# Optimization experiments

Measured on AMD Instinct MI355X. Metric: run time of the kernel, lower is better.

## Reference

```python
import jax, jax.numpy as jnp
import numpy as np

B, L_DEC, L_ENC = 4, 1024, 1024
D_MODEL, D_INNER, N_HEAD, D_K, D_V = 512, 256, 8, 64, 64
TEMP = D_K ** 0.5
EPS = 1e-6


def _layernorm(x, g, b):
    mu = jnp.mean(x, axis=-1, keepdims=True)
    var = jnp.mean(jnp.square(x - mu), axis=-1, keepdims=True)
    return (x - mu) * jax.lax.rsqrt(var + EPS) * g + b


def _mha(x_q, x_kv, Wq, Wk, Wv, Wfc, ln_g, ln_b, mask):
    # Faithful to source: only the query input is layer-normed; k/v use raw x_kv.
    resid = x_q
    qn = _layernorm(x_q, ln_g, ln_b)
    # Stacked per-head projections: Wq/Wk/Wv are [H, d_k, d_model]
    q = jnp.einsum('bld,hkd->bhlk', qn, Wq) / TEMP   # [B,H,Lq,dk]
    k = jnp.einsum('bld,hkd->bhlk', x_kv, Wk)        # [B,H,Lk,dk]
    v = jnp.einsum('bld,hkd->bhlk', x_kv, Wv)        # [B,H,Lk,dv]
    scores = jnp.einsum('bhqd,bhkd->bhqk', q, k)     # [B,H,Lq,Lk]
    if mask is not None:
        scores = jnp.where(mask[:, None, :, :] == 0, -jnp.inf, scores)
    attn = jax.nn.softmax(scores, axis=-1)
    out = jnp.einsum('bhqk,bhkd->bhqd', attn, v)     # [B,H,Lq,dv]
    Bq, H, Lq, dv = out.shape
    out = out.transpose(0, 2, 1, 3).reshape(Bq, Lq, H * dv)
    return out @ Wfc.T + resid


def _ffn(x, W1, b1, W2, b2, ln_g, ln_b):
    resid = x
    h = _layernorm(x, ln_g, ln_b)
    h = jax.nn.relu(h @ W1.T + b1) @ W2.T + b2
    return h + resid


def setup_inputs() -> dict:
    key = jax.random.key(0)
    ks = jax.random.split(key, 20)
    s = 0.02
    dec_input = jax.random.normal(ks[0], (B, L_DEC, D_MODEL), jnp.float32)
    enc_output = jax.random.normal(ks[1], (B, L_ENC, D_MODEL), jnp.float32)
    slf_attn_mask = jnp.tril(jnp.ones((1, L_DEC, L_DEC), jnp.int32))  # causal
    p = {}
    for i, pre in enumerate(['slf', 'enc']):
        base = 2 + i * 4
        p[f'{pre}_Wq'] = jax.random.normal(ks[base], (N_HEAD, D_K, D_MODEL), jnp.float32) * s
        p[f'{pre}_Wk'] = jax.random.normal(ks[base + 1], (N_HEAD, D_K, D_MODEL), jnp.float32) * s
        p[f'{pre}_Wv'] = jax.random.normal(ks[base + 2], (N_HEAD, D_V, D_MODEL), jnp.float32) * s
        p[f'{pre}_Wfc'] = jax.random.normal(ks[base + 3], (D_MODEL, N_HEAD * D_V), jnp.float32) * s
        p[f'{pre}_ln_g'] = jnp.ones((D_MODEL,), jnp.float32)
        p[f'{pre}_ln_b'] = jnp.zeros((D_MODEL,), jnp.float32)
    p['ffn_W1'] = jax.random.normal(ks[10], (D_INNER, D_MODEL), jnp.float32) * s
    p['ffn_b1'] = jnp.zeros((D_INNER,), jnp.float32)
    p['ffn_W2'] = jax.random.normal(ks[11], (D_MODEL, D_INNER), jnp.float32) * s
    p['ffn_b2'] = jnp.zeros((D_MODEL,), jnp.float32)
    p['ffn_ln_g'] = jnp.ones((D_MODEL,), jnp.float32)
    p['ffn_ln_b'] = jnp.zeros((D_MODEL,), jnp.float32)
    return {'dec_input': dec_input, 'enc_output': enc_output,
            'slf_attn_mask': slf_attn_mask, **p}


def reference(dec_input, enc_output,
              slf_Wq, slf_Wk, slf_Wv, slf_Wfc, slf_ln_g, slf_ln_b,
              enc_Wq, enc_Wk, enc_Wv, enc_Wfc, enc_ln_g, enc_ln_b,
              ffn_W1, ffn_b1, ffn_W2, ffn_b2, ffn_ln_g, ffn_ln_b,
              slf_attn_mask):
    x = _mha(dec_input, dec_input, slf_Wq, slf_Wk, slf_Wv, slf_Wfc,
             slf_ln_g, slf_ln_b, slf_attn_mask)
    x = _mha(x, enc_output, enc_Wq, enc_Wk, enc_Wv, enc_Wfc,
             enc_ln_g, enc_ln_b, None)
    x = _ffn(x, ffn_W1, ffn_b1, ffn_W2, ffn_b2, ffn_ln_g, ffn_ln_b)
    return x
```

## Files before the change

kernel.cpp:

```cpp
#include <hip/hip_runtime.h>
#include <hip/hip_bf16.h>
#include <math.h>

#define DMODEL 512
#define NHEAD  8
#define DHEAD  64

typedef __attribute__((ext_vector_type(8))) short bf16x8;
typedef __attribute__((ext_vector_type(4))) float f32x4;
typedef __attribute__((ext_vector_type(16))) float f32x16;
typedef __attribute__((ext_vector_type(4))) short short4v;
typedef __attribute__((ext_vector_type(4))) unsigned int u32x4;

static __device__ inline short f2bf(float f) {
    __hip_bfloat16 h = __float2bfloat16(f);
    return *reinterpret_cast<short*>(&h);
}

#define GLOAD_LDS16(gp, lp)                                                      \
    __builtin_amdgcn_global_load_lds(                                            \
        (const __attribute__((address_space(1))) unsigned int*)(gp),             \
        (__attribute__((address_space(3))) unsigned int*)(lp), 16, 0, 0)

struct CvtArgs {
    const float* src[12];
    short*       dst[12];
    int          n[12];
};

__global__ __launch_bounds__(256) void cvt_kernel(CvtArgs args) {
    int t = blockIdx.y;
    int idx = (blockIdx.x * 256 + threadIdx.x) * 8;
    if (idx >= args.n[t]) return;
    const float* s = args.src[t] + idx;
    float4 a = *(const float4*)s;
    float4 b = *(const float4*)(s + 4);
    bf16x8 o;
    o[0] = f2bf(a.x); o[1] = f2bf(a.y); o[2] = f2bf(a.z); o[3] = f2bf(a.w);
    o[4] = f2bf(b.x); o[5] = f2bf(b.y); o[6] = f2bf(b.z); o[7] = f2bf(b.w);
    *(bf16x8*)(args.dst[t] + idx) = o;
}

__global__ __launch_bounds__(256) void ln_kernel(const float* __restrict__ X,
                                                 const float* __restrict__ gam,
                                                 const float* __restrict__ bet,
                                                 short* __restrict__ Y) {
    int row = blockIdx.x * 4 + (threadIdx.x >> 6);
    int tid = threadIdx.x & 63;
    const float* x = X + (size_t)row * DMODEL;
    float4 a = *(const float4*)(x + tid * 4);
    float4 b = *(const float4*)(x + 256 + tid * 4);
    float sum = a.x + a.y + a.z + a.w + b.x + b.y + b.z + b.w;
    float sq  = a.x*a.x + a.y*a.y + a.z*a.z + a.w*a.w
              + b.x*b.x + b.y*b.y + b.z*b.z + b.w*b.w;
#pragma unroll
    for (int off = 1; off < 64; off <<= 1) {
        sum += __shfl_xor(sum, off);
        sq  += __shfl_xor(sq, off);
    }
    float mu  = sum * (1.0f / DMODEL);
    float var = sq * (1.0f / DMODEL) - mu * mu;
    float r   = rsqrtf(var + 1e-6f);

    float4 g1 = *(const float4*)(gam + tid * 4);
    float4 c1 = *(const float4*)(bet + tid * 4);
    float4 g2 = *(const float4*)(gam + 256 + tid * 4);
    float4 c2 = *(const float4*)(bet + 256 + tid * 4);
    short4v y1, y2;
    y1.x = f2bf((a.x - mu) * r * g1.x + c1.x);
    y1.y = f2bf((a.y - mu) * r * g1.y + c1.y);
    y1.z = f2bf((a.z - mu) * r * g1.z + c1.z);
    y1.w = f2bf((a.w - mu) * r * g1.w + c1.w);
    y2.x = f2bf((b.x - mu) * r * g2.x + c2.x);
    y2.y = f2bf((b.y - mu) * r * g2.y + c2.y);
    y2.z = f2bf((b.z - mu) * r * g2.z + c2.z);
    y2.w = f2bf((b.w - mu) * r * g2.w + c2.w);
    short* y = Y + (size_t)row * DMODEL;
    *(short4v*)(y + tid * 4)       = y1;
    *(short4v*)(y + 256 + tid * 4) = y2;
}

struct GJobs {
    const short* A[3];
    const short* W[3];
    const float* bias[3];
    const float* resid[3];
    void*        C[3];
    int M[3], N[3], K[3];
    float scale[3];
    int relu[3], obf[3], nblk[3];
};

__global__ __launch_bounds__(256) void gemm_bf16(GJobs jb) {
    __shared__ short As[64 * 64];
    __shared__ short Bs[64 * 64];

    int bid = blockIdx.x, j = 0;
    while (j < 2 && bid >= jb.nblk[j]) { bid -= jb.nblk[j]; ++j; }
    const short* __restrict__ A = jb.A[j];
    const short* __restrict__ W = jb.W[j];
    const int N = jb.N[j], K = jb.K[j];
    const int nbx = N >> 6;
    const int tn = (bid % nbx) * 64;
    const int tm = (bid / nbx) * 64;

    const int tid  = threadIdx.x;
    const int w    = tid >> 6;
    const int l    = tid & 63;
    const int lq   = l & 15;
    const int g    = l >> 4;
    const int wm   = (w >> 1) * 32;
    const int wn   = (w & 1) * 32;
    const int lrow = l >> 3;
    const int lsl  = l & 7;

    f32x4 acc[2][2];
#pragma unroll
    for (int i = 0; i < 2; ++i)
#pragma unroll
        for (int jj = 0; jj < 2; ++jj)
            acc[i][jj] = (f32x4){0.f, 0.f, 0.f, 0.f};

#pragma unroll 1
    for (int k0 = 0; k0 < K; k0 += 64) {
        __syncthreads();
#pragma unroll
        for (int i = 0; i < 2; ++i) {
            int row = i * 32 + w * 8 + lrow;
            int slot = lsl ^ (row & 7);
            GLOAD_LDS16(A + (size_t)(tm + row) * K + k0 + slot * 8,
                        As + i * 2048 + w * 512);
            GLOAD_LDS16(W + (size_t)(tn + row) * K + k0 + slot * 8,
                        Bs + i * 2048 + w * 512);
        }
        __syncthreads();

#pragma unroll
        for (int ks = 0; ks < 2; ++ks) {
            const int sl = ((ks * 4 + g) ^ (lq & 7)) * 8;
            bf16x8 af[2], bfv[2];
#pragma unroll
            for (int i = 0; i < 2; ++i) {
                af[i]  = *(const bf16x8*)&As[(wm + i * 16 + lq) * 64 + sl];
                bfv[i] = *(const bf16x8*)&Bs[(wn + i * 16 + lq) * 64 + sl];
            }
#pragma unroll
            for (int i = 0; i < 2; ++i)
#pragma unroll
                for (int jj = 0; jj < 2; ++jj)
                    acc[i][jj] = __builtin_amdgcn_mfma_f32_16x16x32_bf16(
                        af[i], bfv[jj], acc[i][jj], 0, 0, 0);
        }
    }

    const float* bias  = jb.bias[j];
    const float* resid = jb.resid[j];
    const float scale  = jb.scale[j];
    const int relu = jb.relu[j], obf = jb.obf[j];
#pragma unroll
    for (int i = 0; i < 2; ++i) {
#pragma unroll
        for (int r = 0; r < 4; ++r) {
            int row = tm + wm + i * 16 + g * 4 + r;
#pragma unroll
            for (int jj = 0; jj < 2; ++jj) {
                int col = tn + wn + jj * 16 + lq;
                float v = acc[i][jj][r] * scale;
                if (bias)  v += bias[col];
                if (resid) v += resid[(size_t)row * N + col];
                if (relu)  v = fmaxf(v, 0.f);
                if (obf) ((short*)jb.C[j])[(size_t)row * N + col] = f2bf(v);
                else     ((float*)jb.C[j])[(size_t)row * N + col] = v;
            }
        }
    }
}

__global__ __launch_bounds__(128) void attn_mfma_kernel(
        const short* __restrict__ Q, const short* __restrict__ K,
        const short* __restrict__ V, short* __restrict__ O,
        int Lq, int Lk, int causal, int qs, int kvs) {
    __shared__ short Kt[2][64 * 64];
    __shared__ short Vt[2][64 * 72];

    const int tid  = threadIdx.x;
    const int wave = tid >> 6;
    const int lane = tid & 63;
    const int lr   = lane & 31;
    const int h    = lane >> 5;
    const int bh   = blockIdx.y;
    const int b = bh >> 3, hd = bh & 7;
    int qx = blockIdx.x;
    if (blockIdx.y & 16) qx = gridDim.x - 1 - qx;
    const int q0w = qx * 64 + wave * 32;
    const int qg  = q0w + lr;

    bf16x8 qf[4];
    {
        size_t qoff = (size_t)(b * Lq + qg) * qs + hd * DHEAD + h * 8;
#pragma unroll
        for (int ks = 0; ks < 4; ++ks)
            qf[ks] = *(const bf16x8*)(Q + qoff + ks * 16);
    }

    f32x16 o0, o1;
#pragma unroll
    for (int i = 0; i < 16; ++i) { o0[i] = 0.f; o1[i] = 0.f; }
    float ltot = 0.f;

    const int nkt  = causal ? (qx + 1) : (Lk >> 6);
    const int lrow = lane >> 3, lsl = lane & 7;
    const int va = tid & 31, vq = tid >> 5;
    const size_t kvh = (size_t)(b * Lk) * kvs + hd * DHEAD;

    {
#pragma unroll
        for (int i = 0; i < 4; ++i) {
            int row = i * 16 + wave * 8 + lrow;
            GLOAD_LDS16(K + kvh + (size_t)row * kvs + (lsl ^ lrow) * 8,
                        &Kt[0][i * 1024 + wave * 512]);
        }
#pragma unroll
        for (int d2 = 0; d2 < 2; ++d2) {
            size_t gb = kvh + (size_t)(2 * va) * kvs + vq * 8 + d2 * 32;
            bf16x8 v0 = *(const bf16x8*)(V + gb);
            bf16x8 v1 = *(const bf16x8*)(V + gb + kvs);
#pragma unroll
            for (int i = 0; i < 8; ++i)
                *(unsigned*)&Vt[0][(vq * 8 + d2 * 32 + i) * 72 + 2 * va] =
                    (unsigned)(unsigned short)v0[i] |
                    ((unsigned)(unsigned short)v1[i] << 16);
        }
    }
    __syncthreads();

#pragma unroll 1
    for (int kt = 0; kt < nkt; ++kt) {
        const int cur = kt & 1, nxt = cur ^ 1;
        const short* KT = Kt[cur];
        const short* VT = Vt[cur];
        const int havenext = (kt + 1 < nkt);
        bf16x8 vn0a, vn0b, vn1a, vn1b;
        if (havenext) {
            const size_t kb = kvh + (size_t)((kt + 1) * 64) * kvs;
#pragma unroll
            for (int i = 0; i < 4; ++i) {
                int row = i * 16 + wave * 8 + lrow;
                GLOAD_LDS16(K + kb + (size_t)row * kvs + (lsl ^ lrow) * 8,
                            &Kt[nxt][i * 1024 + wave * 512]);
            }
            size_t gb = kb + (size_t)(2 * va) * kvs + vq * 8;
            vn0a = *(const bf16x8*)(V + gb);
            vn0b = *(const bf16x8*)(V + gb + kvs);
            vn1a = *(const bf16x8*)(V + gb + 32);
            vn1b = *(const bf16x8*)(V + gb + kvs + 32);
        }

        f32x16 s0, s1;
#pragma unroll
        for (int i = 0; i < 16; ++i) { s0[i] = 0.f; s1[i] = 0.f; }
#pragma unroll
        for (int ks = 0; ks < 4; ++ks) {
            const int sl = ((ks * 2 + h) ^ (lr & 7)) * 8;
            bf16x8 kf0 = *(const bf16x8*)&KT[lr * 64 + sl];
            bf16x8 kf1 = *(const bf16x8*)&KT[(32 + lr) * 64 + sl];
            s0 = __builtin_amdgcn_mfma_f32_32x32x16_bf16(kf0, qf[ks], s0, 0, 0, 0);
            s1 = __builtin_amdgcn_mfma_f32_32x32x16_bf16(kf1, qf[ks], s1, 0, 0, 0);
        }

        const int needmask = causal && (kt * 64 + 63 > q0w);
        bf16x8 pa[4];
#pragma unroll
        for (int st = 0; st < 2; ++st) {
            float e[16];
#pragma unroll
            for (int r = 0; r < 16; ++r) {
                float sv = st ? s1[r] : s0[r];
                if (needmask) {
                    int kg = kt * 64 + st * 32 + (r & 3) + 8 * (r >> 2) + 4 * h;
                    if (kg > qg) sv = -1e30f;
                }
                float ev = __expf(fminf(sv, 60.f));
                e[r] = ev;
                ltot += ev;
            }
            unsigned w[8], x[8];
#pragma unroll
            for (int i = 0; i < 8; ++i)
                w[i] = (unsigned)(unsigned short)f2bf(e[2 * i]) |
                       ((unsigned)(unsigned short)f2bf(e[2 * i + 1]) << 16);
#pragma unroll
            for (int i = 0; i < 8; ++i)
                x[i] = (unsigned)__shfl_xor((int)w[i], 32);
            u32x4 f0, f1;
            f0[0] = h ? x[2] : w[0];  f0[1] = h ? x[3] : w[1];
            f0[2] = h ? w[2] : x[0];  f0[3] = h ? w[3] : x[1];
            f1[0] = h ? x[6] : w[4];  f1[1] = h ? x[7] : w[5];
            f1[2] = h ? w[6] : x[4];  f1[3] = h ? w[7] : x[5];
            pa[st * 2]     = __builtin_bit_cast(bf16x8, f0);
            pa[st * 2 + 1] = __builtin_bit_cast(bf16x8, f1);
        }

#pragma unroll
        for (int ks = 0; ks < 4; ++ks) {
            const int vo = ks * 16 + h * 8;
            bf16x8 vf0 = *(const bf16x8*)&VT[lr * 72 + vo];
            bf16x8 vf1 = *(const bf16x8*)&VT[(32 + lr) * 72 + vo];
            o0 = __builtin_amdgcn_mfma_f32_32x32x16_bf16(pa[ks], vf0, o0, 0, 0, 0);
            o1 = __builtin_amdgcn_mfma_f32_32x32x16_bf16(pa[ks], vf1, o1, 0, 0, 0);
        }

        if (havenext) {
#pragma unroll
            for (int i = 0; i < 8; ++i) {
                *(unsigned*)&Vt[nxt][(vq * 8 + i) * 72 + 2 * va] =
                    (unsigned)(unsigned short)vn0a[i] |
                    ((unsigned)(unsigned short)vn0b[i] << 16);
                *(unsigned*)&Vt[nxt][(vq * 8 + 32 + i) * 72 + 2 * va] =
                    (unsigned)(unsigned short)vn1a[i] |
                    ((unsigned)(unsigned short)vn1b[i] << 16);
            }
        }
        __syncthreads();
    }

    ltot += __shfl_xor(ltot, 32);
    const size_t ob = (size_t)(b * Lq + q0w) * qs + hd * DHEAD + lr;
#pragma unroll
    for (int r = 0; r < 16; ++r) {
        int row = (r & 3) + 8 * (r >> 2) + 4 * h;
        float lv = __shfl(ltot, row);
        float inv = 1.f / lv;
        O[ob + (size_t)row * qs]      = f2bf(o0[r] * inv);
        O[ob + (size_t)row * qs + 32] = f2bf(o1[r] * inv);
    }
}

static void launch_gemm(GJobs& jb, int njobs, hipStream_t stream) {
    int total = 0;
    for (int i = 0; i < 3; ++i) { if (i >= njobs) jb.nblk[i] = 0; total += jb.nblk[i]; }
    gemm_bf16<<<total, 256, 0, stream>>>(jb);
}

extern "C" void kernel_launch(void* const* d_in, const int* in_sizes, int n_in,
                              void* d_out, int out_size, void* d_ws, size_t ws_size,
                              hipStream_t stream) {
    const float* dec       = (const float*)d_in[0];
    const float* enc       = (const float*)d_in[1];
    const float* slf_Wq    = (const float*)d_in[3];
    const float* slf_Wk    = (const float*)d_in[4];
    const float* slf_Wv    = (const float*)d_in[5];
    const float* slf_Wfc   = (const float*)d_in[6];
    const float* slf_ln_g  = (const float*)d_in[7];
    const float* slf_ln_b  = (const float*)d_in[8];
    const float* enc_Wq    = (const float*)d_in[9];
    const float* enc_Wk    = (const float*)d_in[10];
    const float* enc_Wv    = (const float*)d_in[11];
    const float* enc_Wfc   = (const float*)d_in[12];
    const float* enc_ln_g  = (const float*)d_in[13];
    const float* enc_ln_b  = (const float*)d_in[14];
    const float* ffn_W1    = (const float*)d_in[15];
    const float* ffn_b1    = (const float*)d_in[16];
    const float* ffn_W2    = (const float*)d_in[17];
    const float* ffn_b2    = (const float*)d_in[18];
    const float* ffn_ln_g  = (const float*)d_in[19];
    const float* ffn_ln_b  = (const float*)d_in[20];
    float* out = (float*)d_out;

    const int Bb = 4, L = 1024, M = Bb * L;
    const size_t NE = (size_t)M * DMODEL;
    const int WQN = NHEAD * DHEAD * DMODEL;
    float* ws = (float*)d_ws;
    float* x1 = ws;
    float* x2 = ws + NE;
    short* kv16e = (short*)x2;
    short* sb = (short*)(ws + 2 * NE);
    short* dec16 = sb;               sb += NE;
    short* enc16 = sb;               sb += NE;
    short* qn16  = sb;               sb += NE;
    short* q16   = sb;               sb += NE;
    short* ao16  = sb;               sb += NE;
    short* kv16  = sb;               sb += 2 * NE;
    short* h16   = sb;               sb += NE / 2;
    short* wq_s  = sb;               sb += WQN;
    short* wkv_s = sb;               sb += 2 * WQN;
    short* wfc_s = sb;               sb += WQN;
    short* wq_e  = sb;               sb += WQN;
    short* wkv_e = sb;               sb += 2 * WQN;
    short* wfc_e = sb;               sb += WQN;
    short* w1_16 = sb;               sb += 256 * DMODEL;
    short* w2_16 = sb;               sb += DMODEL * 256;

    CvtArgs ca;
    ca.src[0] = dec;     ca.dst[0] = dec16;         ca.n[0] = (int)NE;
    ca.src[1] = enc;     ca.dst[1] = enc16;         ca.n[1] = (int)NE;
    ca.src[2] = slf_Wq;  ca.dst[2] = wq_s;          ca.n[2] = WQN;
    ca.src[3] = slf_Wk;  ca.dst[3] = wkv_s;         ca.n[3] = WQN;
    ca.src[4] = slf_Wv;  ca.dst[4] = wkv_s + WQN;   ca.n[4] = WQN;
    ca.src[5] = slf_Wfc; ca.dst[5] = wfc_s;         ca.n[5] = WQN;
    ca.src[6] = enc_Wq;  ca.dst[6] = wq_e;          ca.n[6] = WQN;
    ca.src[7] = enc_Wk;  ca.dst[7] = wkv_e;         ca.n[7] = WQN;
    ca.src[8] = enc_Wv;  ca.dst[8] = wkv_e + WQN;   ca.n[8] = WQN;
    ca.src[9] = enc_Wfc; ca.dst[9] = wfc_e;         ca.n[9] = WQN;
    ca.src[10] = ffn_W1; ca.dst[10] = w1_16;        ca.n[10] = 256 * DMODEL;
    ca.src[11] = ffn_W2; ca.dst[11] = w2_16;        ca.n[11] = DMODEL * 256;
    cvt_kernel<<<dim3(1024, 12), 256, 0, stream>>>(ca);

    dim3 attn_grid(L / 64, Bb * NHEAD);
    const int NB512  = (M / 64) * (512 / 64);
    const int NB1024 = (M / 64) * (1024 / 64);
    const int NB256  = (M / 64) * (256 / 64);

    ln_kernel<<<M / 4, 256, 0, stream>>>(dec, slf_ln_g, slf_ln_b, qn16);
    {
        GJobs jb = {};
        jb.A[0] = qn16;  jb.W[0] = wq_s;  jb.C[0] = q16;
        jb.M[0] = M; jb.N[0] = 512;  jb.K[0] = 512; jb.scale[0] = 0.125f;
        jb.obf[0] = 1; jb.nblk[0] = NB512;
        jb.A[1] = dec16; jb.W[1] = wkv_s; jb.C[1] = kv16;
        jb.M[1] = M; jb.N[1] = 1024; jb.K[1] = 512; jb.scale[1] = 1.f;
        jb.obf[1] = 1; jb.nblk[1] = NB1024;
        jb.A[2] = enc16; jb.W[2] = wkv_e; jb.C[2] = kv16e;
        jb.M[2] = M; jb.N[2] = 1024; jb.K[2] = 512; jb.scale[2] = 1.f;
        jb.obf[2] = 1; jb.nblk[2] = NB1024;
        launch_gemm(jb, 3, stream);
    }
    attn_mfma_kernel<<<attn_grid, 128, 0, stream>>>(q16, kv16, kv16 + 512, ao16,
                                                    L, L, 1, DMODEL, 1024);
    {
        GJobs jb = {};
        jb.A[0] = ao16; jb.W[0] = wfc_s; jb.resid[0] = dec; jb.C[0] = x1;
        jb.M[0] = M; jb.N[0] = 512; jb.K[0] = 512; jb.scale[0] = 1.f;
        jb.obf[0] = 0; jb.nblk[0] = NB512;
        launch_gemm(jb, 1, stream);
    }

    ln_kernel<<<M / 4, 256, 0, stream>>>(x1, enc_ln_g, enc_ln_b, qn16);
    {
        GJobs jb = {};
        jb.A[0] = qn16; jb.W[0] = wq_e; jb.C[0] = q16;
        jb.M[0] = M; jb.N[0] = 512; jb.K[0] = 512; jb.scale[0] = 0.125f;
        jb.obf[0] = 1; jb.nblk[0] = NB512;
        launch_gemm(jb, 1, stream);
    }
    attn_mfma_kernel<<<attn_grid, 128, 0, stream>>>(q16, kv16e, kv16e + 512, ao16,
                                                    L, L, 0, DMODEL, 1024);
    {
        GJobs jb = {};
        jb.A[0] = ao16; jb.W[0] = wfc_e; jb.resid[0] = x1; jb.C[0] = x2;
        jb.M[0] = M; jb.N[0] = 512; jb.K[0] = 512; jb.scale[0] = 1.f;
        jb.obf[0] = 0; jb.nblk[0] = NB512;
        launch_gemm(jb, 1, stream);
    }

    ln_kernel<<<M / 4, 256, 0, stream>>>(x2, ffn_ln_g, ffn_ln_b, qn16);
    {
        GJobs jb = {};
        jb.A[0] = qn16; jb.W[0] = w1_16; jb.bias[0] = ffn_b1; jb.C[0] = h16;
        jb.M[0] = M; jb.N[0] = 256; jb.K[0] = 512; jb.scale[0] = 1.f;
        jb.relu[0] = 1; jb.obf[0] = 1; jb.nblk[0] = NB256;
        launch_gemm(jb, 1, stream);
    }
    {
        GJobs jb = {};
        jb.A[0] = h16; jb.W[0] = w2_16; jb.bias[0] = ffn_b2; jb.resid[0] = x2;
        jb.C[0] = out;
        jb.M[0] = M; jb.N[0] = 512; jb.K[0] = 256; jb.scale[0] = 1.f;
        jb.obf[0] = 0; jb.nblk[0] = NB512;
        launch_gemm(jb, 1, stream);
    }
}
```

Before: 280.4 us.

## Split attention over KV ranges with fp32 partials and a combine kernel

Attention blocks now cover 128 queries with 4 waves and are further split along the key dimension into S chunks chosen from available workspace. Each split writes unnormalized fp32 partial outputs and row sums, and a new combine kernel sums them, normalizes, and writes bf16. This raises grid parallelism and evens out the causal load imbalance, at the cost of extra fp32 global traffic, an extra launch per attention, and a per-tile skip check for fully masked waves.

```diff
diff --git a/kernel.cpp b/kernel.cpp
--- a/kernel.cpp
+++ b/kernel.cpp
@@ -176,10 +176,11 @@
     }
 }
 
-__global__ __launch_bounds__(128) void attn_mfma_kernel(
+__global__ __launch_bounds__(256) void attn_mfma_kernel(
         const short* __restrict__ Q, const short* __restrict__ K,
-        const short* __restrict__ V, short* __restrict__ O,
-        int Lq, int Lk, int causal, int qs, int kvs) {
+        const short* __restrict__ V, float* __restrict__ Opart,
+        float* __restrict__ Lpart,
+        int Lq, int Lk, int causal, int qs, int kvs, int S) {
     __shared__ short Kt[2][64 * 64];
     __shared__ short Vt[2][64 * 72];
 
@@ -190,9 +191,9 @@
     const int h    = lane >> 5;
     const int bh   = blockIdx.y;
     const int b = bh >> 3, hd = bh & 7;
-    int qx = blockIdx.x;
-    if (blockIdx.y & 16) qx = gridDim.x - 1 - qx;
-    const int q0w = qx * 64 + wave * 32;
+    const int qx = blockIdx.x;
+    const int sp = blockIdx.z;
+    const int q0w = qx * 128 + wave * 32;
     const int qg  = q0w + lr;
 
     bf16x8 qf[4];
@@ -208,132 +209,158 @@
     for (int i = 0; i < 16; ++i) { o0[i] = 0.f; o1[i] = 0.f; }
     float ltot = 0.f;
 
-    const int nkt  = causal ? (qx + 1) : (Lk >> 6);
+    const int nkt_all = causal ? (2 * qx + 2) : (Lk >> 6);
+    const int klo = (sp * nkt_all) / S;
+    const int khi = ((sp + 1) * nkt_all) / S;
     const int lrow = lane >> 3, lsl = lane & 7;
     const int va = tid & 31, vq = tid >> 5;
     const size_t kvh = (size_t)(b * Lk) * kvs + hd * DHEAD;
 
-    {
-#pragma unroll
-        for (int i = 0; i < 4; ++i) {
-            int row = i * 16 + wave * 8 + lrow;
-            GLOAD_LDS16(K + kvh + (size_t)row * kvs + (lsl ^ lrow) * 8,
-                        &Kt[0][i * 1024 + wave * 512]);
-        }
-#pragma unroll
-        for (int d2 = 0; d2 < 2; ++d2) {
-            size_t gb = kvh + (size_t)(2 * va) * kvs + vq * 8 + d2 * 32;
+    if (klo < khi) {
+        {
+            const size_t kb = kvh + (size_t)(klo * 64) * kvs;
+#pragma unroll
+            for (int i = 0; i < 2; ++i) {
+                int row = wave * 16 + i * 8 + lrow;
+                GLOAD_LDS16(K + kb + (size_t)row * kvs + (lsl ^ lrow) * 8,
+                            &Kt[0][wave * 1024 + i * 512]);
+            }
+            size_t gb = kb + (size_t)(2 * va) * kvs + vq * 8;
             bf16x8 v0 = *(const bf16x8*)(V + gb);
             bf16x8 v1 = *(const bf16x8*)(V + gb + kvs);
 #pragma unroll
             for (int i = 0; i < 8; ++i)
-                *(unsigned*)&Vt[0][(vq * 8 + d2 * 32 + i) * 72 + 2 * va] =
+                *(unsigned*)&Vt[0][(vq * 8 + i) * 72 + 2 * va] =
                     (unsigned)(unsigned short)v0[i] |
                     ((unsigned)(unsigned short)v1[i] << 16);
         }
-    }
-    __syncthreads();
+        __syncthreads();
 
 #pragma unroll 1
-    for (int kt = 0; kt < nkt; ++kt) {
-        const int cur = kt & 1, nxt = cur ^ 1;
-        const short* KT = Kt[cur];
-        const short* VT = Vt[cur];
-        const int havenext = (kt + 1 < nkt);
-        bf16x8 vn0a, vn0b, vn1a, vn1b;
-        if (havenext) {
-            const size_t kb = kvh + (size_t)((kt + 1) * 64) * kvs;
-#pragma unroll
-            for (int i = 0; i < 4; ++i) {
-                int row = i * 16 + wave * 8 + lrow;
-                GLOAD_LDS16(K + kb + (size_t)row * kvs + (lsl ^ lrow) * 8,
-                            &Kt[nxt][i * 1024 + wave * 512]);
+        for (int kt = klo; kt < khi; ++kt) {
+            const int cur = (kt - klo) & 1, nxt = cur ^ 1;
+            const short* KT = Kt[cur];
+            const short* VT = Vt[cur];
+            const int havenext = (kt + 1 < khi);
+            bf16x8 vna, vnb;
+            if (havenext) {
+                const size_t kb = kvh + (size_t)((kt + 1) * 64) * kvs;
+#pragma unroll
+                for (int i = 0; i < 2; ++i) {
+                    int row = wave * 16 + i * 8 + lrow;
+                    GLOAD_LDS16(K + kb + (size_t)row * kvs + (lsl ^ lrow) * 8,
+                                &Kt[nxt][wave * 1024 + i * 512]);
+                }
+                size_t gb = kb + (size_t)(2 * va) * kvs + vq * 8;
+                vna = *(const bf16x8*)(V + gb);
+                vnb = *(const bf16x8*)(V + gb + kvs);
             }
-            size_t gb = kb + (size_t)(2 * va) * kvs + vq * 8;
-            vn0a = *(const bf16x8*)(V + gb);
-            vn0b = *(const bf16x8*)(V + gb + kvs);
-            vn1a = *(const bf16x8*)(V + gb + 32);
-            vn1b = *(const bf16x8*)(V + gb + kvs + 32);
+
+            if (!(causal && kt * 64 > q0w + 31)) {
+                f32x16 s0, s1;
+#pragma unroll
+                for (int i = 0; i < 16; ++i) { s0[i] = 0.f; s1[i] = 0.f; }
+#pragma unroll
+                for (int ks = 0; ks < 4; ++ks) {
+                    const int sl = ((ks * 2 + h) ^ (lr & 7)) * 8;
+                    bf16x8 kf0 = *(const bf16x8*)&KT[lr * 64 + sl];
+                    bf16x8 kf1 = *(const bf16x8*)&KT[(32 + lr) * 64 + sl];
+                    s0 = __builtin_amdgcn_mfma_f32_32x32x16_bf16(kf0, qf[ks], s0, 0, 0, 0);
+                    s1 = __builtin_amdgcn_mfma_f32_32x32x16_bf16(kf1, qf[ks], s1, 0, 0, 0);
+                }
+
+                const int needmask = causal && (kt * 64 + 63 > q0w);
+                bf16x8 pa[4];
+#pragma unroll
+                for (int st = 0; st < 2; ++st) {
+                    float e[16];
+#pragma unroll
+                    for (int r = 0; r < 16; ++r) {
+                        float sv = st ? s1[r] : s0[r];
+                        if (needmask) {
+                            int kg = kt * 64 + st * 32 + (r & 3) + 8 * (r >> 2) + 4 * h;
+                            if (kg > qg) sv = -1e30f;
+                        }
+                        float ev = __expf(fminf(sv, 60.f));
+                        e[r] = ev;
+                        ltot += ev;
+                    }
+                    unsigned w[8], x[8];
+#pragma unroll
+                    for (int i = 0; i < 8; ++i)
+                        w[i] = (unsigned)(unsigned short)f2bf(e[2 * i]) |
+                               ((unsigned)(unsigned short)f2bf(e[2 * i + 1]) << 16);
+#pragma unroll
+                    for (int i = 0; i < 8; ++i)
+                        x[i] = (unsigned)__shfl_xor((int)w[i], 32);
+                    u32x4 f0, f1;
+                    f0[0] = h ? x[2] : w[0];  f0[1] = h ? x[3] : w[1];
+                    f0[2] = h ? w[2] : x[0];  f0[3] = h ? w[3] : x[1];
+                    f1[0] = h ? x[6] : w[4];  f1[1] = h ? x[7] : w[5];
+                    f1[2] = h ? w[6] : x[4];  f1[3] = h ? w[7] : x[5];
+                    pa[st * 2]     = __builtin_bit_cast(bf16x8, f0);
+                    pa[st * 2 + 1] = __builtin_bit_cast(bf16x8, f1);
+                }
+
+#pragma unroll
+                for (int ks = 0; ks < 4; ++ks) {
+                    const int vo = ks * 16 + h * 8;
+                    bf16x8 vf0 = *(const bf16x8*)&VT[lr * 72 + vo];
+                    bf16x8 vf1 = *(const bf16x8*)&VT[(32 + lr) * 72 + vo];
+                    o0 = __builtin_amdgcn_mfma_f32_32x32x16_bf16(pa[ks], vf0, o0, 0, 0, 0);
+                    o1 = __builtin_amdgcn_mfma_f32_32x32x16_bf16(pa[ks], vf1, o1, 0, 0, 0);
+                }
+            }
+
+            if (havenext) {
+#pragma unroll
+                for (int i = 0; i < 8; ++i)
+                    *(unsigned*)&Vt[nxt][(vq * 8 + i) * 72 + 2 * va] =
+                        (unsigned)(unsigned short)vna[i] |
+                        ((unsigned)(unsigned short)vnb[i] << 16);
+            }
+            __syncthreads();
         }
-
-        f32x16 s0, s1;
-#pragma unroll
-        for (int i = 0; i < 16; ++i) { s0[i] = 0.f; s1[i] = 0.f; }
-#pragma unroll
-        for (int ks = 0; ks < 4; ++ks) {
-            const int sl = ((ks * 2 + h) ^ (lr & 7)) * 8;
-            bf16x8 kf0 = *(const bf16x8*)&KT[lr * 64 + sl];
-            bf16x8 kf1 = *(const bf16x8*)&KT[(32 + lr) * 64 + sl];
-            s0 = __builtin_amdgcn_mfma_f32_32x32x16_bf16(kf0, qf[ks], s0, 0, 0, 0);
-            s1 = __builtin_amdgcn_mfma_f32_32x32x16_bf16(kf1, qf[ks], s1, 0, 0, 0);
-        }
-
-        const int needmask = causal && (kt * 64 + 63 > q0w);
-        bf16x8 pa[4];
-#pragma unroll
-        for (int st = 0; st < 2; ++st) {
-            float e[16];
-#pragma unroll
-            for (int r = 0; r < 16; ++r) {
-                float sv = st ? s1[r] : s0[r];
-                if (needmask) {
-                    int kg = kt * 64 + st * 32 + (r & 3) + 8 * (r >> 2) + 4 * h;
-                    if (kg > qg) sv = -1e30f;
-                }
-                float ev = __expf(fminf(sv, 60.f));
-                e[r] = ev;
-                ltot += ev;
-            }
-            unsigned w[8], x[8];
-#pragma unroll
-            for (int i = 0; i < 8; ++i)
-                w[i] = (unsigned)(unsigned short)f2bf(e[2 * i]) |
-                       ((unsigned)(unsigned short)f2bf(e[2 * i + 1]) << 16);
-#pragma unroll
-            for (int i = 0; i < 8; ++i)
-                x[i] = (unsigned)__shfl_xor((int)w[i], 32);
-            u32x4 f0, f1;
-            f0[0] = h ? x[2] : w[0];  f0[1] = h ? x[3] : w[1];
-            f0[2] = h ? w[2] : x[0];  f0[3] = h ? w[3] : x[1];
-            f1[0] = h ? x[6] : w[4];  f1[1] = h ? x[7] : w[5];
-            f1[2] = h ? w[6] : x[4];  f1[3] = h ? w[7] : x[5];
-            pa[st * 2]     = __builtin_bit_cast(bf16x8, f0);
-            pa[st * 2 + 1] = __builtin_bit_cast(bf16x8, f1);
-        }
-
-#pragma unroll
-        for (int ks = 0; ks < 4; ++ks) {
-            const int vo = ks * 16 + h * 8;
-            bf16x8 vf0 = *(const bf16x8*)&VT[lr * 72 + vo];
-            bf16x8 vf1 = *(const bf16x8*)&VT[(32 + lr) * 72 + vo];
-            o0 = __builtin_amdgcn_mfma_f32_32x32x16_bf16(pa[ks], vf0, o0, 0, 0, 0);
-            o1 = __builtin_amdgcn_mfma_f32_32x32x16_bf16(pa[ks], vf1, o1, 0, 0, 0);
-        }
-
-        if (havenext) {
-#pragma unroll
-            for (int i = 0; i < 8; ++i) {
-                *(unsigned*)&Vt[nxt][(vq * 8 + i) * 72 + 2 * va] =
-                    (unsigned)(unsigned short)vn0a[i] |
-                    ((unsigned)(unsigned short)vn0b[i] << 16);
-                *(unsigned*)&Vt[nxt][(vq * 8 + 32 + i) * 72 + 2 * va] =
-                    (unsigned)(unsigned short)vn1a[i] |
-                    ((unsigned)(unsigned short)vn1b[i] << 16);
-            }
-        }
-        __syncthreads();
     }
 
     ltot += __shfl_xor(ltot, 32);
-    const size_t ob = (size_t)(b * Lq + q0w) * qs + hd * DHEAD + lr;
+    float* opw = Opart + (((size_t)sp * gridDim.y + bh) * Lq + q0w) * 64;
 #pragma unroll
     for (int r = 0; r < 16; ++r) {
         int row = (r & 3) + 8 * (r >> 2) + 4 * h;
-        float lv = __shfl(ltot, row);
-        float inv = 1.f / lv;
-        O[ob + (size_t)row * qs]      = f2bf(o0[r] * inv);
-        O[ob + (size_t)row * qs + 32] = f2bf(o1[r] * inv);
-    }
+        opw[(size_t)row * 64 + lr]      = o0[r];
+        opw[(size_t)row * 64 + 32 + lr] = o1[r];
+    }
+    if (h == 0)
+        Lpart[((size_t)sp * gridDim.y + bh) * Lq + q0w + lr] = ltot;
+}
+
+__global__ __launch_bounds__(256) void attn_combine(
+        const float* __restrict__ Opart, const float* __restrict__ Lpart,
+        short* __restrict__ O, int S) {
+    const int BH = 32, L = 1024;
+    int t  = blockIdx.x * 256 + threadIdx.x;
+    int d8 = (t & 7) * 8;
+    int q  = (t >> 3) & (L - 1);
+    int bh = t >> 13;
+    int b = bh >> 3, hd = bh & 7;
+    f32x4 a0 = {0.f, 0.f, 0.f, 0.f}, a1 = {0.f, 0.f, 0.f, 0.f};
+    float l = 0.f;
+    for (int sp = 0; sp < S; ++sp) {
+        const float* p = Opart + (((size_t)sp * BH + bh) * L + q) * 64 + d8;
+        a0 += *(const f32x4*)p;
+        a1 += *(const f32x4*)(p + 4);
+        l  += Lpart[((size_t)sp * BH + bh) * L + q];
+    }
+    float inv = 1.f / l;
+    short* o = O + ((size_t)(b * L + q)) * DMODEL + hd * DHEAD + d8;
+    short4v y0, y1;
+    y0.x = f2bf(a0[0] * inv); y0.y = f2bf(a0[1] * inv);
+    y0.z = f2bf(a0[2] * inv); y0.w = f2bf(a0[3] * inv);
+    y1.x = f2bf(a1[0] * inv); y1.y = f2bf(a1[1] * inv);
+    y1.z = f2bf(a1[2] * inv); y1.w = f2bf(a1[3] * inv);
+    *(short4v*)o       = y0;
+    *(short4v*)(o + 4) = y1;
 }
 
 static void launch_gemm(GJobs& jb, int njobs, hipStream_t stream) {
@@ -391,6 +418,15 @@
     short* w1_16 = sb;               sb += 256 * DMODEL;
     short* w2_16 = sb;               sb += DMODEL * 256;
 
+    size_t used = (size_t)((char*)sb - (char*)d_ws);
+    used = (used + 255) & ~(size_t)255;
+    const size_t per_split = (size_t)32 * L * 64 * 4 + (size_t)32 * L * 4;
+    int S = 1;
+    if (ws_size >= used + 4 * per_split)      S = 4;
+    else if (ws_size >= used + 2 * per_split) S = 2;
+    float* Opart = (float*)((char*)d_ws + used);
+    float* Lpart = Opart + (size_t)S * 32 * L * 64;
+
     CvtArgs ca;
     ca.src[0] = dec;     ca.dst[0] = dec16;         ca.n[0] = (int)NE;
     ca.src[1] = enc;     ca.dst[1] = enc16;         ca.n[1] = (int)NE;
@@ -406,7 +442,8 @@
     ca.src[11] = ffn_W2; ca.dst[11] = w2_16;        ca.n[11] = DMODEL * 256;
     cvt_kernel<<<dim3(1024, 12), 256, 0, stream>>>(ca);
 
-    dim3 attn_grid(L / 64, Bb * NHEAD);
+    dim3 attn_grid(L / 128, Bb * NHEAD, S);
+    const int ncomb = (32 * L * 8) / 256;
     const int NB512  = (M / 64) * (512 / 64);
     const int NB1024 = (M / 64) * (1024 / 64);
     const int NB256  = (M / 64) * (256 / 64);
@@ -425,8 +462,10 @@
         jb.obf[2] = 1; jb.nblk[2] = NB1024;
         launch_gemm(jb, 3, stream);
     }
-    attn_mfma_kernel<<<attn_grid, 128, 0, stream>>>(q16, kv16, kv16 + 512, ao16,
-                                                    L, L, 1, DMODEL, 1024);
+    attn_mfma_kernel<<<attn_grid, 256, 0, stream>>>(q16, kv16, kv16 + 512,
+                                                    Opart, Lpart, L, L, 1,
+                                                    DMODEL, 1024, S);
+    attn_combine<<<ncomb, 256, 0, stream>>>(Opart, Lpart, ao16, S);
     {
         GJobs jb = {};
         jb.A[0] = ao16; jb.W[0] = wfc_s; jb.resid[0] = dec; jb.C[0] = x1;
@@ -443,8 +482,10 @@
         jb.obf[0] = 1; jb.nblk[0] = NB512;
         launch_gemm(jb, 1, stream);
     }
-    attn_mfma_kernel<<<attn_grid, 128, 0, stream>>>(q16, kv16e, kv16e + 512, ao16,
-                                                    L, L, 0, DMODEL, 1024);
+    attn_mfma_kernel<<<attn_grid, 256, 0, stream>>>(q16, kv16e, kv16e + 512,
+                                                    Opart, Lpart, L, L, 0,
+                                                    DMODEL, 1024, S);
+    attn_combine<<<ncomb, 256, 0, stream>>>(Opart, Lpart, ao16, S);
     {
         GJobs jb = {};
         jb.A[0] = ao16; jb.W[0] = wfc_e; jb.resid[0] = x1; jb.C[0] = x2;
```

Measured after the change: 273.7 us. 2.4% less time.
